# Kernel tuning notes

Measured on AMD Instinct MI355X. Metric: run time of the kernel, lower is better.

The kernel has to match this reference:

```python
import jax, jax.numpy as jnp
import numpy as np

D_MODEL = 2048
NUM_HEADS = 32
NUM_KV_HEADS = 8
D_K = 64
N_PER_KV = NUM_HEADS // NUM_KV_HEADS  # 4
B, S = 1, 2048


def setup_inputs() -> dict:
    key = jax.random.key(0)
    ks = jax.random.split(key, 11)
    sc = 0.02
    return {
        "q": jax.random.normal(ks[0], (B, S, D_MODEL), jnp.float32),
        "k": jax.random.normal(ks[1], (B, S, D_MODEL), jnp.float32),
        "v": jax.random.normal(ks[2], (B, S, D_MODEL), jnp.float32),
        "mask": jnp.ones((1, 1, S, S), jnp.bool_),
        # linear weights stored as [in, out] so y = x @ W + b
        "wq": jax.random.normal(ks[3], (D_MODEL, NUM_HEADS * D_K), jnp.float32) * sc,
        "bq": jnp.zeros((NUM_HEADS * D_K,), jnp.float32),
        "wk": jax.random.normal(ks[4], (D_MODEL, NUM_KV_HEADS * D_K), jnp.float32) * sc,
        "bk": jnp.zeros((NUM_KV_HEADS * D_K,), jnp.float32),
        "wv": jax.random.normal(ks[5], (D_MODEL, NUM_KV_HEADS * D_K), jnp.float32) * sc,
        "bv": jnp.zeros((NUM_KV_HEADS * D_K,), jnp.float32),
        "wo": jax.random.normal(ks[6], (D_MODEL, D_MODEL), jnp.float32) * sc,
        "bo": jnp.zeros((D_MODEL,), jnp.float32),
    }


def reference(q, k, v, mask, wq, bq, wk, bk, wv, bv, wo, bo):
    b, s, _ = q.shape
    # projections
    qh = (q @ wq + bq).reshape(b, s, NUM_HEADS, D_K).transpose(0, 2, 1, 3)      # [b,h,s,d]
    kh = (k @ wk + bk).reshape(b, s, NUM_KV_HEADS, D_K).transpose(0, 2, 1, 3)   # [b,g,s,d]
    vh = (v @ wv + bv).reshape(b, s, NUM_KV_HEADS, D_K).transpose(0, 2, 1, 3)   # [b,g,s,d]
    # group query heads: head h = g*N_PER_KV + j, matching repeat_interleave of KV
    qg = qh.reshape(b, NUM_KV_HEADS, N_PER_KV, s, D_K)
    scores = jnp.einsum('bgnqd,bgkd->bgnqk', qg, kh) / jnp.sqrt(jnp.float32(D_K))
    scores = scores.reshape(b, NUM_HEADS, s, s)
    scores = jnp.where(mask, scores, jnp.float32(-1e9))
    attn = jax.nn.softmax(scores, axis=-1)                                       # [b,h,s,s]
    out = jnp.einsum('bgnqk,bgkd->bgnqd', attn.reshape(b, NUM_KV_HEADS, N_PER_KV, s, s), vh)
    out = out.reshape(b, NUM_HEADS, s, D_K).transpose(0, 2, 1, 3).reshape(b, s, D_MODEL)
    out = out @ wo + bo
    return out, attn
```

## Files before the change

### kernel.cpp

```cpp
#include <hip/hip_runtime.h>

constexpr int S   = 2048;
constexpr int DM  = 2048;
constexpr int HD  = 64;
constexpr int NH  = 32;
constexpr int NKV = 8;
constexpr int DKV = NKV * HD;

using f32x4  = __attribute__((ext_vector_type(4))) float;
using bf16x8 = __attribute__((ext_vector_type(8))) short;
using s16x4  = __attribute__((ext_vector_type(4))) short;

__device__ __forceinline__ short f2bf(float x) {
  union { float f; unsigned u; } v; v.f = x;
  unsigned r = (v.u + 0x7fffu + ((v.u >> 16) & 1u)) >> 16;
  return (short)r;
}

__device__ __forceinline__ void gld_lds16(void* lds, const void* g) {
  __builtin_amdgcn_global_load_lds(
      (const __attribute__((address_space(1))) unsigned*)g,
      (__attribute__((address_space(3))) unsigned*)lds, 16, 0, 0);
}

template <int NISSUE>
__device__ __forceinline__ void stage128(char* lds, const char* g, size_t gstride) {
  const int tid  = threadIdx.x;
  const int w    = tid >> 6;
  const int lane = tid & 63;
#pragma unroll
  for (int i = 0; i < NISSUE; ++i) {
    const int off = i * 4096 + w * 1024 + lane * 16;
    const int row = off >> 7;
    const int cb  = off & 127;
    gld_lds16(lds + i * 4096 + w * 1024,
              g + (size_t)row * gstride + (cb ^ ((row & 7) << 4)));
  }
}

__global__ __launch_bounds__(256) void cvt_bf16_kernel(
    const float* __restrict__ in, short* __restrict__ out, int n8) {
  const int i = blockIdx.x * 256 + threadIdx.x;
  if (i >= n8) return;
  const f32x4* p = (const f32x4*)in + (size_t)i * 2;
  const f32x4 a = p[0], b = p[1];
  bf16x8 o;
  o[0] = f2bf(a[0]); o[1] = f2bf(a[1]); o[2] = f2bf(a[2]); o[3] = f2bf(a[3]);
  o[4] = f2bf(b[0]); o[5] = f2bf(b[1]); o[6] = f2bf(b[2]); o[7] = f2bf(b[3]);
  *((bf16x8*)out + (size_t)i) = o;
}

__global__ __launch_bounds__(256) void transpose_cvt_kernel(
    const float* __restrict__ src, short* __restrict__ dst, int R, int C) {
  __shared__ float t[64][65];
  const int c0 = blockIdx.x * 64, r0 = blockIdx.y * 64;
  const int tid = threadIdx.x;
#pragma unroll
  for (int i = 0; i < 4; ++i) {
    const int idx = tid + i * 256;
    const int r = idx >> 4, c4 = idx & 15;
    const f32x4 v = *(const f32x4*)(src + (size_t)(r0 + r) * C + c0 + c4 * 4);
    t[r][c4 * 4 + 0] = v[0]; t[r][c4 * 4 + 1] = v[1];
    t[r][c4 * 4 + 2] = v[2]; t[r][c4 * 4 + 3] = v[3];
  }
  __syncthreads();
#pragma unroll
  for (int i = 0; i < 4; ++i) {
    const int idx = tid + i * 256;
    const int cc = idx >> 4, r4 = idx & 15;
    s16x4 o;
    o[0] = f2bf(t[r4 * 4 + 0][cc]); o[1] = f2bf(t[r4 * 4 + 1][cc]);
    o[2] = f2bf(t[r4 * 4 + 2][cc]); o[3] = f2bf(t[r4 * 4 + 3][cc]);
    *(s16x4*)(dst + (size_t)(c0 + cc) * R + r0 + r4 * 4) = o;
  }
}

template <bool BF16_OUT>
__global__ __launch_bounds__(256) void gemm_mfma(
    const short* __restrict__ A, const short* __restrict__ Bt,
    const float* __restrict__ bias, void* __restrict__ Cout,
    int M, int N, int K) {
  __shared__ __align__(16) char As[8192];
  __shared__ __align__(16) char Bs[8192];
  const int tid = threadIdx.x;
  const int w = tid >> 6, lane = tid & 63;
  const int wr = w >> 1, wc = w & 1;
  const int lg = lane >> 4, lr = lane & 15;
  const int m0 = blockIdx.y * 64, n0 = blockIdx.x * 64;
  const char* abase = (const char*)A + ((size_t)m0 * K) * 2;
  const char* bbase = (const char*)Bt + ((size_t)n0 * K) * 2;
  const f32x4 zero4 = {0.f, 0.f, 0.f, 0.f};
  f32x4 acc[2][2] = {{zero4, zero4}, {zero4, zero4}};

  for (int k0 = 0; k0 < K; k0 += 64) {
    __syncthreads();
    stage128<2>(As, abase + (size_t)k0 * 2, (size_t)K * 2);
    stage128<2>(Bs, bbase + (size_t)k0 * 2, (size_t)K * 2);
    __syncthreads();
#pragma unroll
    for (int ka = 0; ka < 2; ++ka) {
      const int kb = (ka * 32 + lg * 8) * 2;
      bf16x8 af[2], bf[2];
#pragma unroll
      for (int m = 0; m < 2; ++m) {
        const int row = wr * 32 + m * 16 + lr;
        af[m] = *(const bf16x8*)(As + row * 128 + (kb ^ ((row & 7) << 4)));
      }
#pragma unroll
      for (int n = 0; n < 2; ++n) {
        const int row = wc * 32 + n * 16 + lr;
        bf[n] = *(const bf16x8*)(Bs + row * 128 + (kb ^ ((row & 7) << 4)));
      }
#pragma unroll
      for (int m = 0; m < 2; ++m)
#pragma unroll
        for (int n = 0; n < 2; ++n)
          acc[m][n] = __builtin_amdgcn_mfma_f32_16x16x32_bf16(af[m], bf[n], acc[m][n], 0, 0, 0);
    }
  }
#pragma unroll
  for (int n = 0; n < 2; ++n) {
    const int col = n0 + wc * 32 + n * 16 + lr;
    const float bb = bias[col];
#pragma unroll
    for (int m = 0; m < 2; ++m) {
#pragma unroll
      for (int r = 0; r < 4; ++r) {
        const int row = m0 + wr * 32 + m * 16 + lg * 4 + r;
        const float vv = acc[m][n][r] + bb;
        if (BF16_OUT) ((short*)Cout)[(size_t)row * N + col] = f2bf(vv);
        else          ((float*)Cout)[(size_t)row * N + col] = vv;
      }
    }
  }
}

__global__ __launch_bounds__(256) void attn_kernel(
    const short* __restrict__ Qp,
    const short* __restrict__ Kp,
    const short* __restrict__ Vt,
    float* __restrict__ attn,
    short* __restrict__ AVb) {
  __shared__ __align__(16) char Qs[8192];
  __shared__ __align__(16) char Ks[8192];
  __shared__ __align__(16) char Vs[8192];
  __shared__ __align__(16) char Ps[4][2304];
  const int tid = threadIdx.x;
  const int w = tid >> 6, lane = tid & 63;
  const int lg = lane >> 4, lr = lane & 15;
  const int h = blockIdx.y;
  const int g = h >> 2;
  const int qi0 = blockIdx.x * 64;

  stage128<2>(Qs, (const char*)Qp + (size_t)qi0 * (DM * 2) + h * (HD * 2), (size_t)DM * 2);
  __syncthreads();
  bf16x8 qa[2];
  {
    const int row = w * 16 + lr;
#pragma unroll
    for (int ka = 0; ka < 2; ++ka) {
      const int kb = (ka * 32 + lg * 8) * 2;
      qa[ka] = *(const bf16x8*)(Qs + row * 128 + (kb ^ ((row & 7) << 4)));
    }
  }

  float m[4], l[4];
#pragma unroll
  for (int r = 0; r < 4; ++r) { m[r] = -1e30f; l[r] = 0.0f; }

  const char* kbase = (const char*)Kp + g * (HD * 2);
  const char* vbase = (const char*)Vt + (size_t)(g * HD) * (S * 2);
  float* attnh = attn + (size_t)h * S * S;
  const f32x4 zero4 = {0.f, 0.f, 0.f, 0.f};

  for (int kt = 0; kt < S / 64; ++kt) {
    __syncthreads();
    stage128<2>(Ks, kbase + (size_t)kt * 64 * (DKV * 2), (size_t)DKV * 2);
    __syncthreads();
    f32x4 c[4] = {zero4, zero4, zero4, zero4};
#pragma unroll
    for (int ka = 0; ka < 2; ++ka) {
      const int kb = (ka * 32 + lg * 8) * 2;
#pragma unroll
      for (int n = 0; n < 4; ++n) {
        const int row = n * 16 + lr;
        const bf16x8 kf = *(const bf16x8*)(Ks + row * 128 + (kb ^ ((row & 7) << 4)));
        c[n] = __builtin_amdgcn_mfma_f32_16x16x32_bf16(qa[ka], kf, c[n], 0, 0, 0);
      }
    }
#pragma unroll
    for (int n = 0; n < 4; ++n) c[n] *= 0.125f;
#pragma unroll
    for (int r = 0; r < 4; ++r) {
      float t0 = fmaxf(fmaxf(c[0][r], c[1][r]), fmaxf(c[2][r], c[3][r]));
#pragma unroll
      for (int d2 = 1; d2 < 16; d2 <<= 1) t0 = fmaxf(t0, __shfl_xor(t0, d2, 64));
      const float mn = fmaxf(m[r], t0);
      float e = __expf(c[0][r] - mn) + __expf(c[1][r] - mn) +
                __expf(c[2][r] - mn) + __expf(c[3][r] - mn);
#pragma unroll
      for (int d2 = 1; d2 < 16; d2 <<= 1) e += __shfl_xor(e, d2, 64);
      l[r] = l[r] * __expf(m[r] - mn) + e;
      m[r] = mn;
    }
  }
  float invl[4];
#pragma unroll
  for (int r = 0; r < 4; ++r) invl[r] = 1.0f / l[r];

  f32x4 oacc[4] = {zero4, zero4, zero4, zero4};
  char* pw = &Ps[w][0];

  for (int kt = 0; kt < S / 64; ++kt) {
    __syncthreads();
    stage128<2>(Ks, kbase + (size_t)kt * 64 * (DKV * 2), (size_t)DKV * 2);
    stage128<2>(Vs, vbase + (size_t)kt * 128, (size_t)S * 2);
    __syncthreads();
    f32x4 c[4] = {zero4, zero4, zero4, zero4};
#pragma unroll
    for (int ka = 0; ka < 2; ++ka) {
      const int kb = (ka * 32 + lg * 8) * 2;
#pragma unroll
      for (int n = 0; n < 4; ++n) {
        const int row = n * 16 + lr;
        const bf16x8 kf = *(const bf16x8*)(Ks + row * 128 + (kb ^ ((row & 7) << 4)));
        c[n] = __builtin_amdgcn_mfma_f32_16x16x32_bf16(qa[ka], kf, c[n], 0, 0, 0);
      }
    }
#pragma unroll
    for (int n = 0; n < 4; ++n) c[n] *= 0.125f;
#pragma unroll
    for (int n = 0; n < 4; ++n) {
#pragma unroll
      for (int r = 0; r < 4; ++r) {
        const float p = __expf(c[n][r] - m[r]) * invl[r];
        const int grow = qi0 + w * 16 + lg * 4 + r;
        __builtin_nontemporal_store(p, attnh + (size_t)grow * S + kt * 64 + n * 16 + lr);
        *(short*)(pw + (lg * 4 + r) * 144 + (n * 16 + lr) * 2) = f2bf(p);
      }
    }
    bf16x8 pa[2];
#pragma unroll
    for (int ka = 0; ka < 2; ++ka)
      pa[ka] = *(const bf16x8*)(pw + lr * 144 + (ka * 32 + lg * 8) * 2);
#pragma unroll
    for (int ka = 0; ka < 2; ++ka) {
      const int kb = (ka * 32 + lg * 8) * 2;
#pragma unroll
      for (int n = 0; n < 4; ++n) {
        const int row = n * 16 + lr;
        const bf16x8 vf = *(const bf16x8*)(Vs + row * 128 + (kb ^ ((row & 7) << 4)));
        oacc[n] = __builtin_amdgcn_mfma_f32_16x16x32_bf16(pa[ka], vf, oacc[n], 0, 0, 0);
      }
    }
  }
#pragma unroll
  for (int n = 0; n < 4; ++n) {
#pragma unroll
    for (int r = 0; r < 4; ++r) {
      const int row = qi0 + w * 16 + lg * 4 + r;
      const int col = h * HD + n * 16 + lr;
      AVb[(size_t)row * DM + col] = f2bf(oacc[n][r]);
    }
  }
}

extern "C" void kernel_launch(void* const* d_in, const int* in_sizes, int n_in,
                              void* d_out, int out_size, void* d_ws, size_t ws_size,
                              hipStream_t stream) {
  const float* q  = (const float*)d_in[0];
  const float* k  = (const float*)d_in[1];
  const float* v  = (const float*)d_in[2];
  const float* wq = (const float*)d_in[4];
  const float* bq = (const float*)d_in[5];
  const float* wk = (const float*)d_in[6];
  const float* bk = (const float*)d_in[7];
  const float* wv = (const float*)d_in[8];
  const float* bv = (const float*)d_in[9];
  const float* wo = (const float*)d_in[10];
  const float* bo = (const float*)d_in[11];

  float* out0 = (float*)d_out;
  float* attn = out0 + (size_t)S * DM;

  constexpr size_t MB = 1024 * 1024;
  char* ws = (char*)d_ws;
  short* XA = (short*)(ws);
  short* WT = (short*)(ws + 8 * MB);
  short* Qp = (short*)(ws + 16 * MB);
  short* Kp = (short*)(ws + 24 * MB);
  float* Vp = (float*)(ws + 26 * MB);
  short* Vt = (short*)(ws + 30 * MB);

  const int n8 = S * DM / 8;
  dim3 cvtg(n8 / 256);

  cvt_bf16_kernel<<<cvtg, 256, 0, stream>>>(q, XA, n8);
  transpose_cvt_kernel<<<dim3(DM / 64, DM / 64), 256, 0, stream>>>(wq, WT, DM, DM);
  gemm_mfma<true><<<dim3(DM / 64, S / 64), 256, 0, stream>>>(XA, WT, bq, Qp, S, DM, DM);
  cvt_bf16_kernel<<<cvtg, 256, 0, stream>>>(k, XA, n8);
  transpose_cvt_kernel<<<dim3(DKV / 64, DM / 64), 256, 0, stream>>>(wk, WT, DM, DKV);
  gemm_mfma<true><<<dim3(DKV / 64, S / 64), 256, 0, stream>>>(XA, WT, bk, Kp, S, DKV, DM);
  cvt_bf16_kernel<<<cvtg, 256, 0, stream>>>(v, XA, n8);
  transpose_cvt_kernel<<<dim3(DKV / 64, DM / 64), 256, 0, stream>>>(wv, WT, DM, DKV);
  gemm_mfma<false><<<dim3(DKV / 64, S / 64), 256, 0, stream>>>(XA, WT, bv, Vp, S, DKV, DM);
  transpose_cvt_kernel<<<dim3(DKV / 64, S / 64), 256, 0, stream>>>(Vp, Vt, S, DKV);

  attn_kernel<<<dim3(S / 64, NH), 256, 0, stream>>>(Qp, Kp, Vt, attn, XA);

  transpose_cvt_kernel<<<dim3(DM / 64, DM / 64), 256, 0, stream>>>(wo, WT, DM, DM);
  gemm_mfma<false><<<dim3(DM / 64, S / 64), 256, 0, stream>>>(XA, WT, bo, out0, S, DM, DM);
}
```

Measured before the change: 872.4 us.

## Double-buffer GEMM and attention tiles, transpose score MFMA, vectorize attn stores

The GEMM kernel gains templated tile sizes, with 128x64 used for the large projections, and double-buffered LDS staging so the next K-slice loads while the current one computes. The attention kernel double-buffers its K/V tiles and swaps the MFMA operands so each lane holds one query row. That lets the softmax statistics be kept per lane and reduced across lanes only once at the end. Probabilities are computed with exp2 and a folded log-sum offset, then written as 16-byte nontemporal vector stores and packed bf16 LDS writes. The risks are higher LDS use per block, which may reduce occupancy, and a more complex indexing scheme.

```diff
diff --git a/kernel.cpp b/kernel.cpp
--- a/kernel.cpp
+++ b/kernel.cpp
@@ -15,6 +15,9 @@
   union { float f; unsigned u; } v; v.f = x;
   unsigned r = (v.u + 0x7fffu + ((v.u >> 16) & 1u)) >> 16;
   return (short)r;
+}
+__device__ __forceinline__ unsigned pack2bf(float a, float b) {
+  return (unsigned)(unsigned short)f2bf(a) | ((unsigned)(unsigned short)f2bf(b) << 16);
 }
 
 __device__ __forceinline__ void gld_lds16(void* lds, const void* g) {
@@ -75,58 +78,69 @@
   }
 }
 
-template <bool BF16_OUT>
+template <int BM, int BN, bool BF16_OUT>
 __global__ __launch_bounds__(256) void gemm_mfma(
     const short* __restrict__ A, const short* __restrict__ Bt,
     const float* __restrict__ bias, void* __restrict__ Cout,
     int M, int N, int K) {
-  __shared__ __align__(16) char As[8192];
-  __shared__ __align__(16) char Bs[8192];
+  constexpr int WM = BM / 2, WN = BN / 2;
+  constexpr int MT = WM / 16, NT = WN / 16;
+  __shared__ __align__(16) char As[2][BM * 128];
+  __shared__ __align__(16) char Bs[2][BN * 128];
   const int tid = threadIdx.x;
   const int w = tid >> 6, lane = tid & 63;
   const int wr = w >> 1, wc = w & 1;
   const int lg = lane >> 4, lr = lane & 15;
-  const int m0 = blockIdx.y * 64, n0 = blockIdx.x * 64;
-  const char* abase = (const char*)A + ((size_t)m0 * K) * 2;
-  const char* bbase = (const char*)Bt + ((size_t)n0 * K) * 2;
-  const f32x4 zero4 = {0.f, 0.f, 0.f, 0.f};
-  f32x4 acc[2][2] = {{zero4, zero4}, {zero4, zero4}};
-
-  for (int k0 = 0; k0 < K; k0 += 64) {
+  const int m0 = blockIdx.y * BM, n0 = blockIdx.x * BN;
+  const char* abase = (const char*)A + (size_t)m0 * K * 2;
+  const char* bbase = (const char*)Bt + (size_t)n0 * K * 2;
+  f32x4 acc[MT][NT];
+#pragma unroll
+  for (int m = 0; m < MT; ++m)
+#pragma unroll
+    for (int n = 0; n < NT; ++n) acc[m][n] = (f32x4){0.f, 0.f, 0.f, 0.f};
+
+  stage128<BM / 32>(As[0], abase, (size_t)K * 2);
+  stage128<BN / 32>(Bs[0], bbase, (size_t)K * 2);
+  __syncthreads();
+  const int NKS = K / 64;
+  for (int ks = 0; ks < NKS; ++ks) {
+    const int cur = ks & 1;
+    if (ks + 1 < NKS) {
+      stage128<BM / 32>(As[cur ^ 1], abase + (size_t)(ks + 1) * 128, (size_t)K * 2);
+      stage128<BN / 32>(Bs[cur ^ 1], bbase + (size_t)(ks + 1) * 128, (size_t)K * 2);
+    }
+#pragma unroll
+    for (int ka = 0; ka < 2; ++ka) {
+      const int kb = ka * 64 + lg * 16;
+      bf16x8 af[MT], bfr[NT];
+#pragma unroll
+      for (int m = 0; m < MT; ++m) {
+        const int row = wr * WM + m * 16 + lr;
+        af[m] = *(const bf16x8*)(As[cur] + row * 128 + (kb ^ ((row & 7) << 4)));
+      }
+#pragma unroll
+      for (int n = 0; n < NT; ++n) {
+        const int row = wc * WN + n * 16 + lr;
+        bfr[n] = *(const bf16x8*)(Bs[cur] + row * 128 + (kb ^ ((row & 7) << 4)));
+      }
+#pragma unroll
+      for (int m = 0; m < MT; ++m)
+#pragma unroll
+        for (int n = 0; n < NT; ++n)
+          acc[m][n] = __builtin_amdgcn_mfma_f32_16x16x32_bf16(af[m], bfr[n], acc[m][n], 0, 0, 0);
+    }
     __syncthreads();
-    stage128<2>(As, abase + (size_t)k0 * 2, (size_t)K * 2);
-    stage128<2>(Bs, bbase + (size_t)k0 * 2, (size_t)K * 2);
-    __syncthreads();
-#pragma unroll
-    for (int ka = 0; ka < 2; ++ka) {
-      const int kb = (ka * 32 + lg * 8) * 2;
-      bf16x8 af[2], bf[2];
-#pragma unroll
-      for (int m = 0; m < 2; ++m) {
-        const int row = wr * 32 + m * 16 + lr;
-        af[m] = *(const bf16x8*)(As + row * 128 + (kb ^ ((row & 7) << 4)));
-      }
-#pragma unroll
-      for (int n = 0; n < 2; ++n) {
-        const int row = wc * 32 + n * 16 + lr;
-        bf[n] = *(const bf16x8*)(Bs + row * 128 + (kb ^ ((row & 7) << 4)));
-      }
-#pragma unroll
-      for (int m = 0; m < 2; ++m)
-#pragma unroll
-        for (int n = 0; n < 2; ++n)
-          acc[m][n] = __builtin_amdgcn_mfma_f32_16x16x32_bf16(af[m], bf[n], acc[m][n], 0, 0, 0);
-    }
-  }
-#pragma unroll
-  for (int n = 0; n < 2; ++n) {
-    const int col = n0 + wc * 32 + n * 16 + lr;
+  }
+#pragma unroll
+  for (int n = 0; n < NT; ++n) {
+    const int col = n0 + wc * WN + n * 16 + lr;
     const float bb = bias[col];
 #pragma unroll
-    for (int m = 0; m < 2; ++m) {
+    for (int m = 0; m < MT; ++m) {
 #pragma unroll
       for (int r = 0; r < 4; ++r) {
-        const int row = m0 + wr * 32 + m * 16 + lg * 4 + r;
+        const int row = m0 + wr * WM + m * 16 + lg * 4 + r;
         const float vv = acc[m][n][r] + bb;
         if (BF16_OUT) ((short*)Cout)[(size_t)row * N + col] = f2bf(vv);
         else          ((float*)Cout)[(size_t)row * N + col] = vv;
@@ -141,118 +155,125 @@
     const short* __restrict__ Vt,
     float* __restrict__ attn,
     short* __restrict__ AVb) {
-  __shared__ __align__(16) char Qs[8192];
-  __shared__ __align__(16) char Ks[8192];
-  __shared__ __align__(16) char Vs[8192];
-  __shared__ __align__(16) char Ps[4][2304];
+  __shared__ __align__(16) char Ks[2][8192];
+  __shared__ __align__(16) char Vs[2][8192];
+  __shared__ __align__(16) char Ps[4][2048];
+  constexpr float SC = 0.125f * 1.44269504f;
   const int tid = threadIdx.x;
   const int w = tid >> 6, lane = tid & 63;
   const int lg = lane >> 4, lr = lane & 15;
   const int h = blockIdx.y;
   const int g = h >> 2;
   const int qi0 = blockIdx.x * 64;
-
-  stage128<2>(Qs, (const char*)Qp + (size_t)qi0 * (DM * 2) + h * (HD * 2), (size_t)DM * 2);
-  __syncthreads();
-  bf16x8 qa[2];
-  {
-    const int row = w * 16 + lr;
-#pragma unroll
-    for (int ka = 0; ka < 2; ++ka) {
-      const int kb = (ka * 32 + lg * 8) * 2;
-      qa[ka] = *(const bf16x8*)(Qs + row * 128 + (kb ^ ((row & 7) << 4)));
-    }
-  }
-
-  float m[4], l[4];
-#pragma unroll
-  for (int r = 0; r < 4; ++r) { m[r] = -1e30f; l[r] = 0.0f; }
+  const int NT = S / 64;
 
   const char* kbase = (const char*)Kp + g * (HD * 2);
   const char* vbase = (const char*)Vt + (size_t)(g * HD) * (S * 2);
   float* attnh = attn + (size_t)h * S * S;
   const f32x4 zero4 = {0.f, 0.f, 0.f, 0.f};
 
-  for (int kt = 0; kt < S / 64; ++kt) {
-    __syncthreads();
-    stage128<2>(Ks, kbase + (size_t)kt * 64 * (DKV * 2), (size_t)DKV * 2);
-    __syncthreads();
+  stage128<2>(Vs[0], (const char*)Qp + (size_t)qi0 * (DM * 2) + h * (HD * 2), (size_t)DM * 2);
+  stage128<2>(Ks[0], kbase, (size_t)DKV * 2);
+  __syncthreads();
+  bf16x8 qb[2];
+  {
+    const int row = w * 16 + lr;
+#pragma unroll
+    for (int ka = 0; ka < 2; ++ka) {
+      const int kb = ka * 64 + lg * 16;
+      qb[ka] = *(const bf16x8*)(Vs[0] + row * 128 + (kb ^ ((row & 7) << 4)));
+    }
+  }
+
+  float m2 = -1e30f, l = 0.f;
+  for (int kt = 0; kt < NT; ++kt) {
+    const int cur = kt & 1;
+    if (kt + 1 < NT)
+      stage128<2>(Ks[cur ^ 1], kbase + (size_t)(kt + 1) * 64 * (DKV * 2), (size_t)DKV * 2);
     f32x4 c[4] = {zero4, zero4, zero4, zero4};
 #pragma unroll
     for (int ka = 0; ka < 2; ++ka) {
-      const int kb = (ka * 32 + lg * 8) * 2;
+      const int kb = ka * 64 + lg * 16;
 #pragma unroll
       for (int n = 0; n < 4; ++n) {
         const int row = n * 16 + lr;
-        const bf16x8 kf = *(const bf16x8*)(Ks + row * 128 + (kb ^ ((row & 7) << 4)));
-        c[n] = __builtin_amdgcn_mfma_f32_16x16x32_bf16(qa[ka], kf, c[n], 0, 0, 0);
-      }
-    }
-#pragma unroll
-    for (int n = 0; n < 4; ++n) c[n] *= 0.125f;
-#pragma unroll
-    for (int r = 0; r < 4; ++r) {
-      float t0 = fmaxf(fmaxf(c[0][r], c[1][r]), fmaxf(c[2][r], c[3][r]));
-#pragma unroll
-      for (int d2 = 1; d2 < 16; d2 <<= 1) t0 = fmaxf(t0, __shfl_xor(t0, d2, 64));
-      const float mn = fmaxf(m[r], t0);
-      float e = __expf(c[0][r] - mn) + __expf(c[1][r] - mn) +
-                __expf(c[2][r] - mn) + __expf(c[3][r] - mn);
-#pragma unroll
-      for (int d2 = 1; d2 < 16; d2 <<= 1) e += __shfl_xor(e, d2, 64);
-      l[r] = l[r] * __expf(m[r] - mn) + e;
-      m[r] = mn;
-    }
-  }
-  float invl[4];
-#pragma unroll
-  for (int r = 0; r < 4; ++r) invl[r] = 1.0f / l[r];
+        const bf16x8 kf = *(const bf16x8*)(Ks[cur] + row * 128 + (kb ^ ((row & 7) << 4)));
+        c[n] = __builtin_amdgcn_mfma_f32_16x16x32_bf16(kf, qb[ka], c[n], 0, 0, 0);
+      }
+    }
+    float t = fmaxf(fmaxf(fmaxf(c[0][0], c[0][1]), fmaxf(c[0][2], c[0][3])),
+                    fmaxf(fmaxf(c[1][0], c[1][1]), fmaxf(c[1][2], c[1][3])));
+    t = fmaxf(t, fmaxf(fmaxf(fmaxf(c[2][0], c[2][1]), fmaxf(c[2][2], c[2][3])),
+                       fmaxf(fmaxf(c[3][0], c[3][1]), fmaxf(c[3][2], c[3][3]))));
+    const float nm = fmaxf(m2, t * SC);
+    float add = 0.f;
+#pragma unroll
+    for (int n = 0; n < 4; ++n)
+#pragma unroll
+      for (int r = 0; r < 4; ++r) add += exp2f(fmaf(c[n][r], SC, -nm));
+    l = fmaf(l, exp2f(m2 - nm), add);
+    m2 = nm;
+    __syncthreads();
+  }
+#pragma unroll
+  for (int d = 16; d <= 32; d <<= 1) {
+    const float om = __shfl_xor(m2, d, 64);
+    const float ol = __shfl_xor(l, d, 64);
+    const float nm = fmaxf(m2, om);
+    l = fmaf(l, exp2f(m2 - nm), ol * exp2f(om - nm));
+    m2 = nm;
+  }
+  const float moff = m2 + __log2f(l);
 
   f32x4 oacc[4] = {zero4, zero4, zero4, zero4};
-  char* pw = &Ps[w][0];
-
-  for (int kt = 0; kt < S / 64; ++kt) {
-    __syncthreads();
-    stage128<2>(Ks, kbase + (size_t)kt * 64 * (DKV * 2), (size_t)DKV * 2);
-    stage128<2>(Vs, vbase + (size_t)kt * 128, (size_t)S * 2);
-    __syncthreads();
+  char* pw = &Ps[w][0] + lr * 128;
+  stage128<2>(Ks[0], kbase, (size_t)DKV * 2);
+  stage128<2>(Vs[0], vbase, (size_t)S * 2);
+  __syncthreads();
+  for (int kt = 0; kt < NT; ++kt) {
+    const int cur = kt & 1;
+    if (kt + 1 < NT) {
+      stage128<2>(Ks[cur ^ 1], kbase + (size_t)(kt + 1) * 64 * (DKV * 2), (size_t)DKV * 2);
+      stage128<2>(Vs[cur ^ 1], vbase + (size_t)(kt + 1) * 128, (size_t)S * 2);
+    }
     f32x4 c[4] = {zero4, zero4, zero4, zero4};
 #pragma unroll
     for (int ka = 0; ka < 2; ++ka) {
-      const int kb = (ka * 32 + lg * 8) * 2;
+      const int kb = ka * 64 + lg * 16;
 #pragma unroll
       for (int n = 0; n < 4; ++n) {
         const int row = n * 16 + lr;
-        const bf16x8 kf = *(const bf16x8*)(Ks + row * 128 + (kb ^ ((row & 7) << 4)));
-        c[n] = __builtin_amdgcn_mfma_f32_16x16x32_bf16(qa[ka], kf, c[n], 0, 0, 0);
-      }
-    }
-#pragma unroll
-    for (int n = 0; n < 4; ++n) c[n] *= 0.125f;
+        const bf16x8 kf = *(const bf16x8*)(Ks[cur] + row * 128 + (kb ^ ((row & 7) << 4)));
+        c[n] = __builtin_amdgcn_mfma_f32_16x16x32_bf16(kf, qb[ka], c[n], 0, 0, 0);
+      }
+    }
 #pragma unroll
     for (int n = 0; n < 4; ++n) {
-#pragma unroll
-      for (int r = 0; r < 4; ++r) {
-        const float p = __expf(c[n][r] - m[r]) * invl[r];
-        const int grow = qi0 + w * 16 + lg * 4 + r;
-        __builtin_nontemporal_store(p, attnh + (size_t)grow * S + kt * 64 + n * 16 + lr);
-        *(short*)(pw + (lg * 4 + r) * 144 + (n * 16 + lr) * 2) = f2bf(p);
-      }
+      f32x4 p;
+#pragma unroll
+      for (int r = 0; r < 4; ++r) p[r] = exp2f(fmaf(c[n][r], SC, -moff));
+      __builtin_nontemporal_store(
+          p, (f32x4*)(attnh + (size_t)(qi0 + w * 16 + lr) * S + kt * 64 + n * 16 + lg * 4));
+      const unsigned long long dv =
+          (unsigned long long)pack2bf(p[0], p[1]) |
+          ((unsigned long long)pack2bf(p[2], p[3]) << 32);
+      *(unsigned long long*)(pw + ((n * 32 + lg * 8) ^ ((lr & 7) << 4))) = dv;
     }
     bf16x8 pa[2];
 #pragma unroll
     for (int ka = 0; ka < 2; ++ka)
-      pa[ka] = *(const bf16x8*)(pw + lr * 144 + (ka * 32 + lg * 8) * 2);
-#pragma unroll
-    for (int ka = 0; ka < 2; ++ka) {
-      const int kb = (ka * 32 + lg * 8) * 2;
+      pa[ka] = *(const bf16x8*)(pw + ((ka * 64 + lg * 16) ^ ((lr & 7) << 4)));
+#pragma unroll
+    for (int ka = 0; ka < 2; ++ka) {
+      const int kb = ka * 64 + lg * 16;
 #pragma unroll
       for (int n = 0; n < 4; ++n) {
         const int row = n * 16 + lr;
-        const bf16x8 vf = *(const bf16x8*)(Vs + row * 128 + (kb ^ ((row & 7) << 4)));
+        const bf16x8 vf = *(const bf16x8*)(Vs[cur] + row * 128 + (kb ^ ((row & 7) << 4)));
         oacc[n] = __builtin_amdgcn_mfma_f32_16x16x32_bf16(pa[ka], vf, oacc[n], 0, 0, 0);
       }
     }
+    __syncthreads();
   }
 #pragma unroll
   for (int n = 0; n < 4; ++n) {
@@ -297,17 +318,17 @@
 
   cvt_bf16_kernel<<<cvtg, 256, 0, stream>>>(q, XA, n8);
   transpose_cvt_kernel<<<dim3(DM / 64, DM / 64), 256, 0, stream>>>(wq, WT, DM, DM);
-  gemm_mfma<true><<<dim3(DM / 64, S / 64), 256, 0, stream>>>(XA, WT, bq, Qp, S, DM, DM);
+  gemm_mfma<128, 64, true><<<dim3(DM / 64, S / 128), 256, 0, stream>>>(XA, WT, bq, Qp, S, DM, DM);
   cvt_bf16_kernel<<<cvtg, 256, 0, stream>>>(k, XA, n8);
   transpose_cvt_kernel<<<dim3(DKV / 64, DM / 64), 256, 0, stream>>>(wk, WT, DM, DKV);
-  gemm_mfma<true><<<dim3(DKV / 64, S / 64), 256, 0, stream>>>(XA, WT, bk, Kp, S, DKV, DM);
+  gemm_mfma<64, 64, true><<<dim3(DKV / 64, S / 64), 256, 0, stream>>>(XA, WT, bk, Kp, S, DKV, DM);
   cvt_bf16_kernel<<<cvtg, 256, 0, stream>>>(v, XA, n8);
   transpose_cvt_kernel<<<dim3(DKV / 64, DM / 64), 256, 0, stream>>>(wv, WT, DM, DKV);
-  gemm_mfma<false><<<dim3(DKV / 64, S / 64), 256, 0, stream>>>(XA, WT, bv, Vp, S, DKV, DM);
+  gemm_mfma<64, 64, false><<<dim3(DKV / 64, S / 64), 256, 0, stream>>>(XA, WT, bv, Vp, S, DKV, DM);
   transpose_cvt_kernel<<<dim3(DKV / 64, S / 64), 256, 0, stream>>>(Vp, Vt, S, DKV);
 
   attn_kernel<<<dim3(S / 64, NH), 256, 0, stream>>>(Qp, Kp, Vt, attn, XA);
 
   transpose_cvt_kernel<<<dim3(DM / 64, DM / 64), 256, 0, stream>>>(wo, WT, DM, DM);
-  gemm_mfma<false><<<dim3(DM / 64, S / 64), 256, 0, stream>>>(XA, WT, bo, out0, S, DM, DM);
-}
+  gemm_mfma<128, 64, false><<<dim3(DM / 64, S / 128), 256, 0, stream>>>(XA, WT, bo, out0, S, DM, DM);
+}
```

After: 860.9 us. About the same (-1.3%).
